# Performance work log

Hardware: AMD Instinct MI355X
Metric: run time of the kernel (lower is better)

Reference implementation:

```python
import jax, jax.numpy as jnp
import numpy as np

K_NBR = 64  # max_num_neighbors in radius()
M1, M2, M3 = 2048, 512, 512  # fps sample counts: 4096*0.5, 2048*0.25, 512*1.0
R1, R2, R3 = 0.2, 0.4, 1.0


def _fps_idx(pos, m):
    # Furthest point sampling, deterministic start at index 0. pos: [N,3] -> idx [m]
    d2 = jnp.sum((pos - pos[0]) ** 2, axis=-1)  # [N]

    def step(min_d2, _):
        nxt = jnp.argmax(min_d2).astype(jnp.int32)
        min_d2 = jnp.minimum(min_d2, jnp.sum((pos - pos[nxt]) ** 2, axis=-1))
        return min_d2, nxt

    _, rest = jax.lax.scan(step, d2, None, length=m - 1)
    return jnp.concatenate([jnp.zeros((1,), jnp.int32), rest])


def _ball_query(pos_src, pos_q, r, k):
    # Nearest up-to-k neighbors within radius r. Returns idx [M,k], valid mask [M,k].
    d2 = (jnp.sum(pos_q ** 2, -1)[:, None] + jnp.sum(pos_src ** 2, -1)[None, :]
          - 2.0 * pos_q @ pos_src.T)  # [M,N]
    neg = jnp.where(d2 <= r * r, -d2, -jnp.inf)
    vals, idx = jax.lax.top_k(neg, k)
    return idx, vals > -jnp.inf


def _sa_layer(x, pos, m, r, w1, b1, w2, b2):
    # x: [B,N,C], pos: [B,N,3] -> (x_new [B,m,Cout], pos_new [B,m,3])
    idx = jax.vmap(lambda p: _fps_idx(p, m))(pos)                     # [B,m]
    pos_q = jnp.take_along_axis(pos, idx[..., None], axis=1)         # [B,m,3]
    nbr, mask = jax.vmap(lambda s, q: _ball_query(s, q, r, K_NBR))(pos, pos_q)
    gather = jax.vmap(lambda a, i: a[i])                              # [N,C],[m,k]->[m,k,C]
    x_j = gather(x, nbr)                                              # [B,m,k,C]
    pos_j = gather(pos, nbr)                                          # [B,m,k,3]
    # PointNetConv message: MLP(concat(x_j, pos_j - pos_i)), max-aggregate
    msg = jnp.concatenate([x_j, pos_j - pos_q[:, :, None, :]], axis=-1)
    h = jnp.maximum(msg @ w1 + b1, 0.0) @ w2 + b2                     # [B,m,k,Cout]
    h = jnp.where(mask[..., None], h, -jnp.inf)
    out = jnp.max(h, axis=2)
    out = jnp.where(jnp.any(mask, axis=2, keepdims=True), out, 0.0)   # empty -> 0
    return out, pos_q


def setup_inputs() -> dict:
    key = jax.random.key(0)
    ks = jax.random.split(key, 8)
    B, N, C3 = 8, 4096, 128
    pos = jax.random.uniform(ks[0], (B, N, 3), jnp.float32)
    batch = jnp.repeat(jnp.arange(B, dtype=jnp.int32)[:, None], N, axis=1)

    def lin(k, ci, co):
        kw, kb = jax.random.split(k)
        s = 1.0 / np.sqrt(ci)
        return (jax.random.uniform(kw, (ci, co), jnp.float32, -s, s),
                jax.random.uniform(kb, (co,), jnp.float32, -s, s))

    w11, b11 = lin(ks[1], 3 + 3, 32)
    w12, b12 = lin(ks[2], 32, 32)
    w21, b21 = lin(ks[3], 32 + 3, 64)
    w22, b22 = lin(ks[4], 64, 64)
    w31, b31 = lin(ks[5], 64 + 3, C3)
    w32, b32 = lin(ks[6], C3, C3)
    return dict(pos=pos, batch=batch,
                w11=w11, b11=b11, w12=w12, b12=b12,
                w21=w21, b21=b21, w22=w22, b22=b22,
                w31=w31, b31=b31, w32=w32, b32=b32)


def reference(pos, batch, w11, b11, w12, b12, w21, b21, w22, b22, w31, b31, w32, b32):
    # Layer 1 uses positions as features (x = pos in encoder forward)
    x1, p1 = _sa_layer(pos, pos, M1, R1, w11, b11, w12, b12)
    x2, p2 = _sa_layer(x1, p1, M2, R2, w21, b21, w22, b22)
    x3, p3 = _sa_layer(x2, p2, M3, R3, w31, b31, w32, b32)
    return x3, p3, batch[:, :M3]
```

## Files before the change

kernel.cpp:

```cpp
#include <hip/hip_runtime.h>
#include <hip/hip_bf16.h>
#include <float.h>

typedef unsigned long long u64;

static __device__ __forceinline__ float d2_rn(float ax, float ay, float az,
                                              float bx, float by, float bz) {
  float dx = __fsub_rn(ax, bx), dy = __fsub_rn(ay, by), dz = __fsub_rn(az, bz);
  return __fadd_rn(__fadd_rn(__fmul_rn(dx, dx), __fmul_rn(dy, dy)), __fmul_rn(dz, dz));
}

static __device__ __forceinline__ void merge2(u64& a1, u64& a2, u64 b1, u64 b2) {
  bool agt = a1 > b1;
  u64 m1 = agt ? a1 : b1;
  u64 lo = agt ? b1 : a1;
  u64 cs = agt ? a2 : b2;
  a1 = m1;
  a2 = lo > cs ? lo : cs;
}

static __device__ __forceinline__ u64 pack_key(float v, int i) {
  if (v < 0.f) return 0ull;
  return ((u64)__float_as_uint(v) << 32) | (unsigned)(~i);
}

template<int CTRL>
static __device__ __forceinline__ u64 dpp_u64(u64 x) {
  unsigned lo = (unsigned)__builtin_amdgcn_update_dpp(0, (int)(unsigned)x, CTRL, 0xF, 0xF, true);
  unsigned hi = (unsigned)__builtin_amdgcn_update_dpp(0, (int)(unsigned)(x >> 32), CTRL, 0xF, 0xF, true);
  return ((u64)hi << 32) | lo;
}

template<int CTRL>
static __device__ __forceinline__ void merge_dpp(u64& a1, u64& a2) {
  u64 b1 = dpp_u64<CTRL>(a1);
  u64 b2 = dpp_u64<CTRL>(a2);
  merge2(a1, a2, b1, b2);
}

static __device__ __forceinline__ void wave_top2_dpp(u64& a1, u64& a2) {
  merge_dpp<0xB1>(a1, a2);
  merge_dpp<0x4E>(a1, a2);
  merge_dpp<0x141>(a1, a2);
  merge_dpp<0x140>(a1, a2);
  merge_dpp<0x142>(a1, a2);
  merge_dpp<0x143>(a1, a2);
}

template<int N, int M, int NPT, int T>
static __device__ void fps_body(const float* __restrict__ P, float* __restrict__ O,
                                char* smem) {
  constexpr int W = T / 64;
  static_assert(N == T * NPT, "layout");
  float* xs = (float*)smem;
  float* ys = xs + N;
  float* zs = ys + N;
  uint4* slots = (uint4*)(zs + N);
  const int tid = threadIdx.x;
  const int lane = tid & 63, wv = tid >> 6;

  for (int j = tid; j < N; j += T) {
    xs[j] = P[3 * j]; ys[j] = P[3 * j + 1]; zs[j] = P[3 * j + 2];
  }
  __syncthreads();

  const float c0x = xs[0], c0y = ys[0], c0z = zs[0];
  if (tid == 0) { O[0] = c0x; O[1] = c0y; O[2] = c0z; }

  float md[NPT], px[NPT], py[NPT], pz[NPT];
  float v1 = -1.f, v2 = -1.f; int i1 = 0, i2 = 0;
  #pragma unroll
  for (int k = 0; k < NPT; ++k) {
    int j = tid + k * T;
    px[k] = xs[j]; py[k] = ys[j]; pz[k] = zs[j];
    float m = d2_rn(px[k], py[k], pz[k], c0x, c0y, c0z);
    md[k] = m;
    if (m > v2) { if (m > v1) { v2=v1; i2=i1; v1=m; i1=j; } else { v2=m; i2=j; } }
  }

  u64 a1 = pack_key(v1, i1), a2 = pack_key(v2, i2);
  wave_top2_dpp(a1, a2);
  if (lane == 63)
    slots[wv] = make_uint4((unsigned)a1, (unsigned)(a1 >> 32),
                           (unsigned)a2, (unsigned)(a2 >> 32));

  int t = 1, phase = 0;
  while (t < M) {
    __syncthreads();
    uint4 s = slots[phase * W + (lane & (W - 1))];
    a1 = ((u64)s.y << 32) | s.x;
    a2 = ((u64)s.w << 32) | s.z;
    merge_dpp<0xB1>(a1, a2);
    merge_dpp<0x4E>(a1, a2);
    merge_dpp<0x141>(a1, a2);

    const int j1 = (int)(~(unsigned)a1);
    const float c1x = xs[j1], c1y = ys[j1], c1z = zs[j1];
    const float v2f = __uint_as_float((unsigned)(a2 >> 32));

    bool hit = false;
    float c2x = 0.f, c2y = 0.f, c2z = 0.f;
    if (t + 1 < M && v2f > 0.f) {
      int j2 = (int)(~(unsigned)a2);
      c2x = xs[j2]; c2y = ys[j2]; c2z = zs[j2];
      float dd = d2_rn(c2x, c2y, c2z, c1x, c1y, c1z);
      hit = (dd >= v2f);
    }

    if (tid == 0) {
      O[3 * t] = c1x; O[3 * t + 1] = c1y; O[3 * t + 2] = c1z;
      if (hit) { O[3 * t + 3] = c2x; O[3 * t + 4] = c2y; O[3 * t + 5] = c2z; }
    }

    v1 = -1.f; v2 = -1.f; i1 = 0; i2 = 0;
    if (hit) {
      #pragma unroll
      for (int k = 0; k < NPT; ++k) {
        float m = md[k];
        m = fminf(m, d2_rn(px[k], py[k], pz[k], c1x, c1y, c1z));
        m = fminf(m, d2_rn(px[k], py[k], pz[k], c2x, c2y, c2z));
        md[k] = m;
        int j = tid + k * T;
        if (m > v2) { if (m > v1) { v2=v1; i2=i1; v1=m; i1=j; } else { v2=m; i2=j; } }
      }
    } else {
      #pragma unroll
      for (int k = 0; k < NPT; ++k) {
        float m = fminf(md[k], d2_rn(px[k], py[k], pz[k], c1x, c1y, c1z));
        md[k] = m;
        int j = tid + k * T;
        if (m > v2) { if (m > v1) { v2=v1; i2=i1; v1=m; i1=j; } else { v2=m; i2=j; } }
      }
    }

    a1 = pack_key(v1, i1); a2 = pack_key(v2, i2);
    wave_top2_dpp(a1, a2);
    if (lane == 63)
      slots[(phase ^ 1) * W + wv] = make_uint4((unsigned)a1, (unsigned)(a1 >> 32),
                                               (unsigned)a2, (unsigned)(a2 >> 32));
    phase ^= 1;
    t += hit ? 2 : 1;
  }
}

template<int N, int M, int NPT>
__global__ __launch_bounds__(512, 2) void fps_kernel(const float* __restrict__ pos,
                                                     float* __restrict__ out) {
  __shared__ __align__(16) char smem[3 * N * 4 + 2 * 8 * 16];
  fps_body<N, M, NPT, 512>(pos + (size_t)blockIdx.x * N * 3,
                           out + (size_t)blockIdx.x * M * 3, smem);
}

template<int C, int H>
__global__ void g_kernel(const float* __restrict__ x, const float* __restrict__ pos,
                         const float* __restrict__ W, float* __restrict__ g, int rows) {
  int idx = blockIdx.x * 256 + threadIdx.x;
  if (idx >= rows * H) return;
  int row = idx / H, h = idx - row * H;
  const float* xr = x + (size_t)row * C;
  const float* pr = pos + (size_t)row * 3;
  float acc = 0.f;
  for (int c = 0; c < C; ++c) acc = fmaf(xr[c], W[c * H + h], acc);
  #pragma unroll
  for (int c = 0; c < 3; ++c) acc = fmaf(pr[c], W[(C + c) * H + h], acc);
  g[idx] = acc;
}

template<int N, int H, int C, int QB>
__global__ __launch_bounds__(256) void sa_kernel(
    const float* __restrict__ src,
    const float* __restrict__ g,
    const float* __restrict__ qpos,
    const float* __restrict__ W2,
    const float* __restrict__ b1v,
    const float* __restrict__ W1p,
    const float* __restrict__ b2v,
    float r2, int M,
    float* __restrict__ out)
{
  constexpr int TPS = C / 2;
  constexpr int SG  = 256 / TPS;
  constexpr int JT  = SG * 4;
  constexpr int STRIDE = JT + 4;
  const int tid = threadIdx.x;
  const int b = blockIdx.y;
  const int sgi = tid / TPS;
  const int c2 = 2 * (tid - sgi * TPS);

  __shared__ __align__(16) __hip_bfloat16 sW2h[H * C];
  __shared__ float sD2[N];
  __shared__ float sT[H];
  __shared__ __align__(16) float sHj[STRIDE * H];
  __shared__ float sScr[512];
  __shared__ int   sNbr[64];
  __shared__ int   sWS[4];
  __shared__ int   sCnt, sNn, sNc, sBin, sBefore;
  __shared__ float sTauV; __shared__ int sTauI;

  int*   sHist  = (int*)sScr;
  float* sCand  = sScr + 256;
  int*   sCandI = (int*)(sScr + 320);
  float* sRed   = sScr;

  const float* srcb = src + (size_t)b * N * 3;
  const float* gb   = g   + (size_t)b * N * H;

  for (int e = tid; e < H * C; e += 256) sW2h[e] = __float2bfloat16(W2[e]);

  for (int qi = 0; qi < QB; ++qi) {
    const int i = blockIdx.x * QB + qi;
    const float* qp = qpos + ((size_t)b * M + i) * 3;
    const float qx = qp[0], qy = qp[1], qz = qp[2];
    const float qq = __fadd_rn(__fadd_rn(__fmul_rn(qx, qx), __fmul_rn(qy, qy)),
                               __fmul_rn(qz, qz));
    if (tid < H)
      sT[tid] = fmaf(qx, W1p[tid], fmaf(qy, W1p[H + tid], fmaf(qz, W1p[2 * H + tid], -b1v[tid])));
    if (tid == 0) { sCnt = 0; sNn = 0; sNc = 0; }
    sHist[tid] = 0;
    __syncthreads();

    int lc = 0;
    for (int j = tid; j < N; j += 256) {
      float sx = srcb[3 * j], sy = srcb[3 * j + 1], sz = srcb[3 * j + 2];
      float ss  = __fadd_rn(__fadd_rn(__fmul_rn(sx, sx), __fmul_rn(sy, sy)), __fmul_rn(sz, sz));
      float dot = __fadd_rn(__fadd_rn(__fmul_rn(qx, sx), __fmul_rn(qy, sy)), __fmul_rn(qz, sz));
      float d2  = __fsub_rn(__fadd_rn(qq, ss), __fmul_rn(2.0f, dot));
      sD2[j] = d2;
      lc += (d2 <= r2) ? 1 : 0;
    }
    #pragma unroll
    for (int off = 32; off > 0; off >>= 1) lc += __shfl_xor(lc, off, 64);
    if ((tid & 63) == 0) atomicAdd(&sCnt, lc);
    __syncthreads();
    const int cnt = sCnt;

    float tauv; int taui;
    if (cnt <= 64) {
      tauv = r2; taui = 0x7fffffff;
    } else {
      const float scale = 256.0f / r2;
      for (int j = tid; j < N; j += 256) {
        float d2 = sD2[j];
        if (d2 <= r2) {
          int bin = (int)(d2 * scale);
          bin = bin < 0 ? 0 : (bin > 255 ? 255 : bin);
          atomicAdd(&sHist[bin], 1);
        }
      }
      __syncthreads();
      int cbin = sHist[tid];
      int lane = tid & 63, wvi = tid >> 6;
      int v = cbin;
      #pragma unroll
      for (int off = 1; off < 64; off <<= 1) {
        int o = __shfl_up(v, off, 64);
        if (lane >= off) v += o;
      }
      if (lane == 63) sWS[wvi] = v;
      __syncthreads();
      int wadd = 0;
      for (int w = 0; w < wvi; ++w) wadd += sWS[w];
      int incl = v + wadd, excl = incl - cbin;
      if (excl < 64 && incl >= 64) { sBin = tid; sBefore = excl; }
      __syncthreads();
      const int bstar = sBin;
      const int kneed = 64 - sBefore;
      for (int j = tid; j < N; j += 256) {
        float d2 = sD2[j];
        if (d2 <= r2) {
          int bin = (int)(d2 * scale);
          bin = bin < 0 ? 0 : (bin > 255 ? 255 : bin);
          if (bin == bstar) {
            int p = atomicAdd(&sNc, 1);
            if (p < 64) { sCand[p] = d2; sCandI[p] = j; }
          }
        }
      }
      __syncthreads();
      if (tid == 0) {
        int nc = sNc < 64 ? sNc : 64;
        for (int a = 1; a < nc; ++a) {
          float dv = sCand[a]; int di = sCandI[a];
          int p = a - 1;
          while (p >= 0 && (sCand[p] > dv || (sCand[p] == dv && sCandI[p] > di))) {
            sCand[p + 1] = sCand[p]; sCandI[p + 1] = sCandI[p]; --p;
          }
          sCand[p + 1] = dv; sCandI[p + 1] = di;
        }
        int kk = (kneed < nc ? kneed : nc) - 1; if (kk < 0) kk = 0;
        sTauV = sCand[kk]; sTauI = sCandI[kk];
      }
      __syncthreads();
      tauv = sTauV; taui = sTauI;
    }

    for (int j = tid; j < N; j += 256) {
      float d2 = sD2[j];
      if (d2 < tauv || (d2 == tauv && j <= taui)) {
        int p = atomicAdd(&sNn, 1);
        if (p < 64) sNbr[p] = j;
      }
    }
    __syncthreads();
    const int nn = sNn < 64 ? sNn : 64;

    float m0 = -FLT_MAX, m1 = -FLT_MAX;
    for (int t0 = 0; t0 < nn; t0 += JT) {
      int jt = nn - t0; if (jt > JT) jt = JT;
      __syncthreads();
      for (int e = tid; e < JT * H; e += 256) {
        int jj = e / H, h = e - jj * H;
        float hv = 0.f;
        if (jj < jt) {
          int j = sNbr[t0 + jj];
          hv = gb[(size_t)j * H + h] - sT[h];
          hv = hv > 0.f ? hv : 0.f;
        }
        sHj[h * STRIDE + jj] = hv;
      }
      __syncthreads();
      float a0 = 0, a1 = 0, a2 = 0, a3 = 0, c0 = 0, c1 = 0, c2a = 0, c3 = 0;
      const int jbase = sgi * 4;
      for (int h = 0; h < H; ++h) {
        float4 hv = *reinterpret_cast<const float4*>(&sHj[h * STRIDE + jbase]);
        __hip_bfloat162 wp = *reinterpret_cast<const __hip_bfloat162*>(&sW2h[h * C + c2]);
        float wx = __bfloat162float(wp.x), wy = __bfloat162float(wp.y);
        a0 = fmaf(hv.x, wx, a0); a1 = fmaf(hv.y, wx, a1);
        a2 = fmaf(hv.z, wx, a2); a3 = fmaf(hv.w, wx, a3);
        c0 = fmaf(hv.x, wy, c0); c1 = fmaf(hv.y, wy, c1);
        c2a = fmaf(hv.z, wy, c2a); c3 = fmaf(hv.w, wy, c3);
      }
      if (jbase + 0 < jt) { m0 = fmaxf(m0, a0); m1 = fmaxf(m1, c0); }
      if (jbase + 1 < jt) { m0 = fmaxf(m0, a1); m1 = fmaxf(m1, c1); }
      if (jbase + 2 < jt) { m0 = fmaxf(m0, a2); m1 = fmaxf(m1, c2a); }
      if (jbase + 3 < jt) { m0 = fmaxf(m0, a3); m1 = fmaxf(m1, c3); }
    }
    __syncthreads();
    sRed[sgi * C + c2]     = m0;
    sRed[sgi * C + c2 + 1] = m1;
    __syncthreads();
    if (tid < TPS) {
      int c = 2 * tid;
      float M0 = sRed[c], M1 = sRed[c + 1];
      #pragma unroll
      for (int s2 = 1; s2 < SG; ++s2) {
        M0 = fmaxf(M0, sRed[s2 * C + c]);
        M1 = fmaxf(M1, sRed[s2 * C + c + 1]);
      }
      float o0 = nn > 0 ? M0 + b2v[c]     : 0.f;
      float o1 = nn > 0 ? M1 + b2v[c + 1] : 0.f;
      float* orow = out + (((size_t)b * M) + i) * C;
      orow[c] = o0; orow[c + 1] = o1;
    }
    __syncthreads();
  }
}

__global__ void tail_kernel(const float* __restrict__ p3, float* __restrict__ d_out) {
  int i = blockIdx.x * 256 + threadIdx.x;
  if (i < 8 * 512 * 3) d_out[524288 + i] = p3[i];
  if (i < 8 * 512)     d_out[536576 + i] = (float)(i >> 9);
}

extern "C" void kernel_launch(void* const* d_in, const int* in_sizes, int n_in,
                              void* d_out, int out_size, void* d_ws, size_t ws_size,
                              hipStream_t stream) {
  (void)in_sizes; (void)n_in; (void)out_size; (void)ws_size;
  const float* pos = (const float*)d_in[0];
  const float* w11 = (const float*)d_in[2];
  const float* b11 = (const float*)d_in[3];
  const float* w12 = (const float*)d_in[4];
  const float* b12 = (const float*)d_in[5];
  const float* w21 = (const float*)d_in[6];
  const float* b21 = (const float*)d_in[7];
  const float* w22 = (const float*)d_in[8];
  const float* b22 = (const float*)d_in[9];
  const float* w31 = (const float*)d_in[10];
  const float* b31 = (const float*)d_in[11];
  const float* w32 = (const float*)d_in[12];
  const float* b32 = (const float*)d_in[13];

  float* ws = (float*)d_ws;
  float* p1 = ws; ws += 8 * 2048 * 3;
  float* p2 = ws; ws += 8 * 512 * 3;
  float* p3 = ws; ws += 8 * 512 * 3;
  float* g1 = ws; ws += 8 * 4096 * 32;
  float* x1 = ws; ws += 8 * 2048 * 32;
  float* g2 = ws; ws += 8 * 2048 * 64;
  float* x2 = ws; ws += 8 * 512 * 64;
  float* g3 = ws; ws += 8 * 512 * 128;
  float* x3 = (float*)d_out;

  fps_kernel<4096, 2048, 8><<<dim3(8), dim3(512), 0, stream>>>(pos, p1);
  g_kernel<3, 32><<<dim3(8 * 4096 * 32 / 256), dim3(256), 0, stream>>>(pos, pos, w11, g1, 8 * 4096);
  sa_kernel<4096, 32, 32, 8><<<dim3(2048 / 8, 8), dim3(256), 0, stream>>>(
      pos, g1, p1, w12, b11, w11 + 3 * 32, b12, 0.04f, 2048, x1);
  fps_kernel<2048, 512, 4><<<dim3(8), dim3(512), 0, stream>>>(p1, p2);
  g_kernel<32, 64><<<dim3(8 * 2048 * 64 / 256), dim3(256), 0, stream>>>(x1, p1, w21, g2, 8 * 2048);
  sa_kernel<2048, 64, 64, 8><<<dim3(512 / 8, 8), dim3(256), 0, stream>>>(
      p1, g2, p2, w22, b21, w21 + 32 * 64, b22, 0.16f, 512, x2);
  fps_kernel<512, 512, 1><<<dim3(8), dim3(512), 0, stream>>>(p2, p3);
  g_kernel<64, 128><<<dim3(8 * 512 * 128 / 256), dim3(256), 0, stream>>>(x2, p2, w31, g3, 8 * 512);
  sa_kernel<512, 128, 128, 8><<<dim3(64, 8), dim3(256), 0, stream>>>(
      p2, g3, p3, w32, b31, w31 + 64 * 128, b32, 1.0f, 512, x3);
  tail_kernel<<<dim3(48), dim3(256), 0, stream>>>(p3, (float*)d_out);
}
```

Measured before the change: 2.436 ms.

## Overlap next-layer FPS with current SA layer in a fused launch

Merges the serial FPS of layer L+1 with the SA (ball query plus MLP) of layer L into one launch. The first 8 blocks run FPS at raised wave priority and the remaining blocks run SA with 512 threads. Because FPS of the next layer only depends on the current layer's positions, its long serial chain can hide behind the SA work. Shared memory is now carved from one dynamic-sized buffer, and the g_kernel launch is moved ahead of FPS. The risk is that the larger 512-thread SA blocks and the bigger shared-memory footprint lower occupancy.

Measured after the change: 2.185 ms. 10.3% less time.

```diff
diff --git a/kernel.cpp b/kernel.cpp
--- a/kernel.cpp
+++ b/kernel.cpp
@@ -166,61 +166,61 @@
   g[idx] = acc;
 }
 
-template<int N, int H, int C, int QB>
-__global__ __launch_bounds__(256) void sa_kernel(
-    const float* __restrict__ src,
-    const float* __restrict__ g,
-    const float* __restrict__ qpos,
-    const float* __restrict__ W2,
-    const float* __restrict__ b1v,
-    const float* __restrict__ W1p,
-    const float* __restrict__ b2v,
-    float r2, int M,
-    float* __restrict__ out)
-{
+template<int N, int H, int C, int T>
+constexpr int sa_smem_bytes() {
+  constexpr int TPS = C / 2, SG = T / TPS, JT = SG * 4, STRIDE = JT + 4;
+  constexpr int SCR = (SG * C > 512) ? SG * C : 512;
+  return H * C * 2 + N * 4 + H * 4 + STRIDE * H * 4 + SCR * 4 + 64 * 4 + 8 * 4 + 8 * 4;
+}
+
+template<int N, int H, int C, int QB, int T>
+static __device__ void sa_body(const float* __restrict__ srcb,
+                               const float* __restrict__ gb,
+                               const float* __restrict__ qposb,
+                               const float* __restrict__ W2, const float* __restrict__ b1v,
+                               const float* __restrict__ W1p, const float* __restrict__ b2v,
+                               float r2, int M, float* __restrict__ outb, int qtile,
+                               char* smem) {
   constexpr int TPS = C / 2;
-  constexpr int SG  = 256 / TPS;
+  constexpr int SG  = T / TPS;
   constexpr int JT  = SG * 4;
   constexpr int STRIDE = JT + 4;
+  constexpr int SCR = (SG * C > 512) ? SG * C : 512;
   const int tid = threadIdx.x;
-  const int b = blockIdx.y;
   const int sgi = tid / TPS;
   const int c2 = 2 * (tid - sgi * TPS);
 
-  __shared__ __align__(16) __hip_bfloat16 sW2h[H * C];
-  __shared__ float sD2[N];
-  __shared__ float sT[H];
-  __shared__ __align__(16) float sHj[STRIDE * H];
-  __shared__ float sScr[512];
-  __shared__ int   sNbr[64];
-  __shared__ int   sWS[4];
-  __shared__ int   sCnt, sNn, sNc, sBin, sBefore;
-  __shared__ float sTauV; __shared__ int sTauI;
+  __hip_bfloat16* sW2h = (__hip_bfloat16*)smem;
+  float* sD2  = (float*)(smem + H * C * 2);
+  float* sT   = sD2 + N;
+  float* sHj  = sT + H;
+  float* sScr = sHj + STRIDE * H;
+  int*   sNbr = (int*)(sScr + SCR);
+  int*   sWS  = sNbr + 64;
+  int*   sIv  = sWS + 8;
+  float* sFv  = (float*)(sIv + 6);
 
   int*   sHist  = (int*)sScr;
   float* sCand  = sScr + 256;
   int*   sCandI = (int*)(sScr + 320);
   float* sRed   = sScr;
 
-  const float* srcb = src + (size_t)b * N * 3;
-  const float* gb   = g   + (size_t)b * N * H;
-
-  for (int e = tid; e < H * C; e += 256) sW2h[e] = __float2bfloat16(W2[e]);
+  for (int e = tid; e < H * C; e += T) sW2h[e] = __float2bfloat16(W2[e]);
 
   for (int qi = 0; qi < QB; ++qi) {
-    const int i = blockIdx.x * QB + qi;
-    const float* qp = qpos + ((size_t)b * M + i) * 3;
+    const int i = qtile * QB + qi;
+    const float* qp = qposb + (size_t)i * 3;
     const float qx = qp[0], qy = qp[1], qz = qp[2];
     const float qq = __fadd_rn(__fadd_rn(__fmul_rn(qx, qx), __fmul_rn(qy, qy)),
                                __fmul_rn(qz, qz));
     if (tid < H)
       sT[tid] = fmaf(qx, W1p[tid], fmaf(qy, W1p[H + tid], fmaf(qz, W1p[2 * H + tid], -b1v[tid])));
-    if (tid == 0) { sCnt = 0; sNn = 0; sNc = 0; }
-    sHist[tid] = 0;
+    if (tid == 0) { sIv[0] = 0; sIv[1] = 0; sIv[2] = 0; }
+    if (tid < 256) sHist[tid] = 0;
     __syncthreads();
 
     int lc = 0;
-    for (int j = tid; j < N; j += 256) {
+    for (int j = tid; j < N; j += T) {
       float sx = srcb[3 * j], sy = srcb[3 * j + 1], sz = srcb[3 * j + 2];
       float ss  = __fadd_rn(__fadd_rn(__fmul_rn(sx, sx), __fmul_rn(sy, sy)), __fmul_rn(sz, sz));
       float dot = __fadd_rn(__fadd_rn(__fmul_rn(qx, sx), __fmul_rn(qy, sy)), __fmul_rn(qz, sz));
@@ -230,16 +230,16 @@
     }
     #pragma unroll
     for (int off = 32; off > 0; off >>= 1) lc += __shfl_xor(lc, off, 64);
-    if ((tid & 63) == 0) atomicAdd(&sCnt, lc);
-    __syncthreads();
-    const int cnt = sCnt;
+    if ((tid & 63) == 0) atomicAdd(&sIv[0], lc);
+    __syncthreads();
+    const int cnt = sIv[0];
 
     float tauv; int taui;
     if (cnt <= 64) {
       tauv = r2; taui = 0x7fffffff;
     } else {
       const float scale = 256.0f / r2;
-      for (int j = tid; j < N; j += 256) {
+      for (int j = tid; j < N; j += T) {
         float d2 = sD2[j];
         if (d2 <= r2) {
           int bin = (int)(d2 * scale);
@@ -248,7 +248,7 @@
         }
       }
       __syncthreads();
-      int cbin = sHist[tid];
+      int cbin = (tid < 256) ? sHist[tid] : 0;
       int lane = tid & 63, wvi = tid >> 6;
       int v = cbin;
       #pragma unroll
@@ -261,24 +261,24 @@
       int wadd = 0;
       for (int w = 0; w < wvi; ++w) wadd += sWS[w];
       int incl = v + wadd, excl = incl - cbin;
-      if (excl < 64 && incl >= 64) { sBin = tid; sBefore = excl; }
-      __syncthreads();
-      const int bstar = sBin;
-      const int kneed = 64 - sBefore;
-      for (int j = tid; j < N; j += 256) {
+      if (tid < 256 && excl < 64 && incl >= 64) { sIv[3] = tid; sIv[4] = excl; }
+      __syncthreads();
+      const int bstar = sIv[3];
+      const int kneed = 64 - sIv[4];
+      for (int j = tid; j < N; j += T) {
         float d2 = sD2[j];
         if (d2 <= r2) {
           int bin = (int)(d2 * scale);
           bin = bin < 0 ? 0 : (bin > 255 ? 255 : bin);
           if (bin == bstar) {
-            int p = atomicAdd(&sNc, 1);
+            int p = atomicAdd(&sIv[2], 1);
             if (p < 64) { sCand[p] = d2; sCandI[p] = j; }
           }
         }
       }
       __syncthreads();
       if (tid == 0) {
-        int nc = sNc < 64 ? sNc : 64;
+        int nc = sIv[2] < 64 ? sIv[2] : 64;
         for (int a = 1; a < nc; ++a) {
           float dv = sCand[a]; int di = sCandI[a];
           int p = a - 1;
@@ -288,27 +288,27 @@
           sCand[p + 1] = dv; sCandI[p + 1] = di;
         }
         int kk = (kneed < nc ? kneed : nc) - 1; if (kk < 0) kk = 0;
-        sTauV = sCand[kk]; sTauI = sCandI[kk];
-      }
-      __syncthreads();
-      tauv = sTauV; taui = sTauI;
-    }
-
-    for (int j = tid; j < N; j += 256) {
+        sFv[0] = sCand[kk]; sIv[5] = sCandI[kk];
+      }
+      __syncthreads();
+      tauv = sFv[0]; taui = sIv[5];
+    }
+
+    for (int j = tid; j < N; j += T) {
       float d2 = sD2[j];
       if (d2 < tauv || (d2 == tauv && j <= taui)) {
-        int p = atomicAdd(&sNn, 1);
+        int p = atomicAdd(&sIv[1], 1);
         if (p < 64) sNbr[p] = j;
       }
     }
     __syncthreads();
-    const int nn = sNn < 64 ? sNn : 64;
+    const int nn = sIv[1] < 64 ? sIv[1] : 64;
 
     float m0 = -FLT_MAX, m1 = -FLT_MAX;
     for (int t0 = 0; t0 < nn; t0 += JT) {
       int jt = nn - t0; if (jt > JT) jt = JT;
       __syncthreads();
-      for (int e = tid; e < JT * H; e += 256) {
+      for (int e = tid; e < JT * H; e += T) {
         int jj = e / H, h = e - jj * H;
         float hv = 0.f;
         if (jj < jt) {
@@ -349,11 +349,49 @@
       }
       float o0 = nn > 0 ? M0 + b2v[c]     : 0.f;
       float o1 = nn > 0 ? M1 + b2v[c + 1] : 0.f;
-      float* orow = out + (((size_t)b * M) + i) * C;
+      float* orow = outb + (size_t)i * C;
       orow[c] = o0; orow[c + 1] = o1;
     }
     __syncthreads();
   }
+}
+
+template<int N, int H, int C, int QB>
+__global__ __launch_bounds__(256) void sa_kernel(
+    const float* __restrict__ src, const float* __restrict__ g,
+    const float* __restrict__ qpos, const float* __restrict__ W2,
+    const float* __restrict__ b1v, const float* __restrict__ W1p,
+    const float* __restrict__ b2v, float r2, int M, float* __restrict__ out) {
+  __shared__ __align__(16) char smem[sa_smem_bytes<N, H, C, 256>()];
+  const int b = blockIdx.y;
+  sa_body<N, H, C, QB, 256>(src + (size_t)b * N * 3, g + (size_t)b * N * H,
+                            qpos + (size_t)b * M * 3, W2, b1v, W1p, b2v, r2, M,
+                            out + (size_t)b * M * C, blockIdx.x, smem);
+}
+
+template<int NF, int MF, int NPTF, int NS, int HS, int CS, int QB, int SAB>
+__global__ __launch_bounds__(512, 2) void fused_kernel(
+    const float* __restrict__ fsrc, float* __restrict__ fdst,
+    const float* __restrict__ src, const float* __restrict__ g,
+    const float* __restrict__ qpos, const float* __restrict__ W2,
+    const float* __restrict__ b1v, const float* __restrict__ W1p,
+    const float* __restrict__ b2v, float r2, int M, float* __restrict__ out) {
+  constexpr int FPS_BYTES = 3 * NF * 4 + 2 * 8 * 16;
+  constexpr int SA_BYTES  = sa_smem_bytes<NS, HS, CS, 512>();
+  constexpr int SMEM = FPS_BYTES > SA_BYTES ? FPS_BYTES : SA_BYTES;
+  __shared__ __align__(16) char smem[SMEM];
+  if (blockIdx.x < 8) {
+    __builtin_amdgcn_s_setprio(3);
+    fps_body<NF, MF, NPTF, 512>(fsrc + (size_t)blockIdx.x * NF * 3,
+                                fdst + (size_t)blockIdx.x * MF * 3, smem);
+    return;
+  }
+  const int bi = blockIdx.x - 8;
+  const int qt = bi % SAB;
+  const int b  = bi / SAB;
+  sa_body<NS, HS, CS, QB, 512>(src + (size_t)b * NS * 3, g + (size_t)b * NS * HS,
+                               qpos + (size_t)b * M * 3, W2, b1v, W1p, b2v, r2, M,
+                               out + (size_t)b * M * CS, qt, smem);
 }
 
 __global__ void tail_kernel(const float* __restrict__ p3, float* __restrict__ d_out) {
@@ -391,17 +429,21 @@
   float* g3 = ws; ws += 8 * 512 * 128;
   float* x3 = (float*)d_out;
 
+  g_kernel<3, 32><<<dim3(8 * 4096 * 32 / 256), dim3(256), 0, stream>>>(pos, pos, w11, g1, 8 * 4096);
   fps_kernel<4096, 2048, 8><<<dim3(8), dim3(512), 0, stream>>>(pos, p1);
-  g_kernel<3, 32><<<dim3(8 * 4096 * 32 / 256), dim3(256), 0, stream>>>(pos, pos, w11, g1, 8 * 4096);
-  sa_kernel<4096, 32, 32, 8><<<dim3(2048 / 8, 8), dim3(256), 0, stream>>>(
-      pos, g1, p1, w12, b11, w11 + 3 * 32, b12, 0.04f, 2048, x1);
-  fps_kernel<2048, 512, 4><<<dim3(8), dim3(512), 0, stream>>>(p1, p2);
+
+  fused_kernel<2048, 512, 4, 4096, 32, 32, 8, 256><<<dim3(8 + 8 * 256), dim3(512), 0, stream>>>(
+      p1, p2, pos, g1, p1, w12, b11, w11 + 3 * 32, b12, 0.04f, 2048, x1);
+
   g_kernel<32, 64><<<dim3(8 * 2048 * 64 / 256), dim3(256), 0, stream>>>(x1, p1, w21, g2, 8 * 2048);
-  sa_kernel<2048, 64, 64, 8><<<dim3(512 / 8, 8), dim3(256), 0, stream>>>(
-      p1, g2, p2, w22, b21, w21 + 32 * 64, b22, 0.16f, 512, x2);
-  fps_kernel<512, 512, 1><<<dim3(8), dim3(512), 0, stream>>>(p2, p3);
+
+  fused_kernel<512, 512, 1, 2048, 64, 64, 8, 64><<<dim3(8 + 8 * 64), dim3(512), 0, stream>>>(
+      p2, p3, p1, g2, p2, w22, b21, w21 + 32 * 64, b22, 0.16f, 512, x2);
+
   g_kernel<64, 128><<<dim3(8 * 512 * 128 / 256), dim3(256), 0, stream>>>(x2, p2, w31, g3, 8 * 512);
+
   sa_kernel<512, 128, 128, 8><<<dim3(64, 8), dim3(256), 0, stream>>>(
       p2, g3, p3, w32, b31, w31 + 64 * 128, b32, 1.0f, 512, x3);
+
   tail_kernel<<<dim3(48), dim3(256), 0, stream>>>(p3, (float*)d_out);
 }
```
